# Kernel optimization log

Measured on AMD Instinct MI355X. Metric: run time of the kernel, lower is better.

The kernel has to match this reference:

```python
import math
import jax, jax.numpy as jnp
import numpy as np

B, T, HIDDEN = 2, 2048, 1024
H, HKV, D = 16, 16, 64


def _rope_tables(T, D):
    inv_freq = 1.0 / (10000.0 ** (jnp.arange(0, D, 2, dtype=jnp.float32) / D))
    t = jnp.arange(T, dtype=jnp.float32)
    freqs = jnp.outer(t, inv_freq)               # [T, D/2]
    emb = jnp.concatenate([freqs, freqs], axis=-1)  # [T, D]
    return jnp.cos(emb), jnp.sin(emb)


def setup_inputs() -> dict:
    key = jax.random.key(0)
    k1, k2, k3 = jax.random.split(key, 3)
    hidden_states = jax.random.normal(k1, (B, T, HIDDEN), dtype=jnp.float32)
    cos, sin = _rope_tables(T, D)
    # trunc-normal-ish init, std = 1/sqrt(fan_in)
    w_qkv = jax.random.normal(k2, ((H + 2 * HKV) * D, HIDDEN), dtype=jnp.float32) / math.sqrt(HIDDEN)
    w_o = jax.random.normal(k3, (HIDDEN, H * D), dtype=jnp.float32) / math.sqrt(H * D)
    return {"hidden_states": hidden_states, "cos": cos, "sin": sin, "w_qkv": w_qkv, "w_o": w_o}


def _rotate_half(x):
    x1, x2 = jnp.split(x, 2, axis=-1)
    return jnp.concatenate([-x2, x1], axis=-1)


def reference(hidden_states, cos, sin, w_qkv, w_o):
    b, t, _ = hidden_states.shape
    # fused QKV projection: [B,T,(H+2*HKV)*D]
    qkv = jnp.einsum('bti,oi->bto', hidden_states, w_qkv)
    qkv = qkv.reshape(b, t, H + 2 * HKV, D)
    q = qkv[:, :, :H]                    # [B,T,H,D]
    k = qkv[:, :, H:H + HKV]             # [B,T,HKV,D]
    v = qkv[:, :, H + HKV:]              # [B,T,HKV,D]
    # inline RoPE; cos/sin broadcast over heads
    c = cos[:, None, :]
    s = sin[:, None, :]
    q = q * c + _rotate_half(q) * s
    k = k * c + _rotate_half(k) * s
    scale = 1.0 / math.sqrt(D)
    attn_scores = jnp.einsum('bthd,bThd->bhtT', q, k) * scale  # [B,H,T,T]
    mask = jnp.tril(jnp.ones((t, t), dtype=bool))
    attn_scores = jnp.where(mask[None, None, :, :], attn_scores, -1e9)
    attn = jax.nn.softmax(attn_scores, axis=-1)
    context = jnp.einsum('bhtT,bThd->bthd', attn, v).reshape(b, t, H * D)
    return jnp.einsum('bti,oi->bto', context, w_o)
```

## Files before the change

kernel.cpp:

```cpp
#include <hip/hip_runtime.h>

typedef __bf16 bf16_t;
typedef __bf16 bf16x4 __attribute__((ext_vector_type(4)));
typedef __bf16 bf16x8 __attribute__((ext_vector_type(8)));
typedef float f32x4 __attribute__((ext_vector_type(4)));
typedef unsigned int u32x2 __attribute__((ext_vector_type(2)));
typedef unsigned long long u64;

#define MFMA16(a, b, c) __builtin_amdgcn_mfma_f32_16x16x32_bf16((a), (b), (c), 0, 0, 0)

#define LDG2LDS16(g, l)                                                        \
    __builtin_amdgcn_global_load_lds(                                          \
        (const __attribute__((address_space(1))) void*)(g),                    \
        (__attribute__((address_space(3))) void*)(l), 16, 0, 0)

#if __has_builtin(__builtin_amdgcn_exp2f)
#define EXP2(x) __builtin_amdgcn_exp2f(x)
#else
#define EXP2(x) exp2f(x)
#endif

__device__ inline bf16x8 load8(const float* p) {
    const f32x4 a = *(const f32x4*)p;
    const f32x4 b = *(const f32x4*)(p + 4);
    bf16x8 r;
#pragma unroll
    for (int i = 0; i < 4; i++) { r[i] = (bf16_t)a[i]; r[4 + i] = (bf16_t)b[i]; }
    return r;
}

__device__ inline u32x2 as2(bf16x4 v) {
    u32x2 r;
    __builtin_memcpy(&r, &v, 8);
    return r;
}

__device__ inline bf16x4 shfl4(bf16x4 v, int src) {
    u64 x;
    __builtin_memcpy(&x, &v, 8);
    x = __shfl(x, src, 64);
    bf16x4 r;
    __builtin_memcpy(&r, &x, 8);
    return r;
}

__global__ __launch_bounds__(256) void convert_kernel(const float* __restrict__ hs,
                                                      const float* __restrict__ wqkv,
                                                      const float* __restrict__ wo,
                                                      bf16_t* __restrict__ outb) {
    const size_t c = ((size_t)blockIdx.x * 256 + threadIdx.x) * 8;
    const float* src;
    size_t off;
    if (c < 4194304) { src = hs; off = c; }
    else if (c < 7340032) { src = wqkv; off = c - 4194304; }
    else { src = wo; off = c - 7340032; }
    *(bf16x8*)(outb + c) = load8(src + off);
}


template <int MODE, int NDIM, int BM>
__global__ __launch_bounds__(256) void gemm_bt(const bf16_t* __restrict__ A,
                                               const bf16_t* __restrict__ B,
                                               float* __restrict__ outp,
                                               bf16_t* __restrict__ q_ws,
                                               bf16_t* __restrict__ k_ws,
                                               bf16_t* __restrict__ v_ws,
                                               const float* __restrict__ cosb,
                                               const float* __restrict__ sinb) {
    constexpr int K = 1024;
    constexpr int IM = BM / 32;
    __shared__ __align__(16) bf16_t As[BM * 32];
    __shared__ __align__(16) bf16_t Bs[128 * 32];

    const int tid = threadIdx.x;
    const int w = tid >> 6;
    const int lane = tid & 63;
    const int lr = lane & 15;
    const int quad = lane >> 4;
    const int m0 = blockIdx.y * BM;
    const int n0 = blockIdx.x * 128;
    const int wm = (w & 1) * (BM / 2);
    const int wn = (w >> 1) * 64;

    const int srow = tid >> 2;
    const int skk = (tid & 3) * 8;
    const bf16_t* gA0 = A + (size_t)(m0 + srow) * K + skk;
    const bf16_t* gA1 = gA0 + (size_t)64 * K;
    const bf16_t* gB0 = B + (size_t)(n0 + srow) * K + skk;
    const bf16_t* gB1 = gB0 + (size_t)64 * K;
    bf16_t* lA0 = As + w * 512;
    bf16_t* lA1 = As + 2048 + w * 512;
    bf16_t* lB0 = Bs + w * 512;
    bf16_t* lB1 = Bs + 2048 + w * 512;

    f32x4 acc[IM][4] = {};

    for (int k0 = 0; k0 < K; k0 += 32) {
        LDG2LDS16(gA0 + k0, lA0);
        if constexpr (BM == 128) LDG2LDS16(gA1 + k0, lA1);
        LDG2LDS16(gB0 + k0, lB0);
        LDG2LDS16(gB1 + k0, lB1);
        __syncthreads();

        bf16x8 af[IM], bfm[4];
#pragma unroll
        for (int im = 0; im < IM; im++)
            af[im] = *(const bf16x8*)&As[(wm + im * 16 + lr) * 32 + quad * 8];
#pragma unroll
        for (int in = 0; in < 4; in++)
            bfm[in] = *(const bf16x8*)&Bs[(wn + in * 16 + lr) * 32 + quad * 8];
#pragma unroll
        for (int im = 0; im < IM; im++)
#pragma unroll
            for (int in = 0; in < 4; in++)
                acc[im][in] = MFMA16(af[im], bfm[in], acc[im][in]);
        __syncthreads();
    }

    if constexpr (MODE == 0) {
#pragma unroll
        for (int im = 0; im < IM; im++)
#pragma unroll
            for (int in = 0; in < 4; in++)
#pragma unroll
                for (int r = 0; r < 4; r++) {
                    const int m = m0 + wm + im * 16 + quad * 4 + r;
                    const int n = n0 + wn + in * 16 + lr;
                    outp[(size_t)m * NDIM + n] = acc[im][in][r];
                }
    } else {
        const int j = (n0 + wn) >> 6;
        if (j < 32) {
            const bool isq = (j < 16);
            const float qs = 0.125f * 1.44269504089f;
#pragma unroll
            for (int im = 0; im < IM; im++) {
#pragma unroll
                for (int r = 0; r < 4; r++) {
                    const int m = m0 + wm + im * 16 + quad * 4 + r;
                    const int b = m >> 11;
                    const int t = m & 2047;
#pragma unroll
                    for (int in = 0; in < 2; in++) {
                        const int d = in * 16 + lr;
                        const float x1 = acc[im][in][r];
                        const float x2 = acc[im][in + 2][r];
                        const float c = cosb[t * 64 + d];
                        const float s = sinb[t * 64 + d];
                        float y1 = x1 * c - x2 * s;
                        float y2 = x2 * c + x1 * s;
                        if (isq) {
                            y1 *= qs; y2 *= qs;
                            const size_t base =
                                ((size_t)(b * 16 + j) * 2048 + t) * 64 + d;
                            q_ws[base] = (bf16_t)y1;
                            q_ws[base + 32] = (bf16_t)y2;
                        } else {
                            const int bh = b * 16 + (j - 16);
                            const size_t off =
                                ((size_t)(bh * 128 + (t >> 4)) * 2) * 512 +
                                ((t & 15) + (d >> 3) * 16) * 8 + (d & 7);
                            k_ws[off] = (bf16_t)y1;
                            k_ws[off + 512] = (bf16_t)y2;
                        }
                    }
                }
            }
        } else {
#pragma unroll
            for (int im = 0; im < IM; im++)
#pragma unroll
                for (int in = 0; in < 4; in++)
#pragma unroll
                    for (int r = 0; r < 4; r++) {
                        const int m = m0 + wm + im * 16 + quad * 4 + r;
                        const int b = m >> 11;
                        const int t = m & 2047;
                        const int d = in * 16 + lr;
                        const int bh = b * 16 + (j - 32);
                        const size_t off =
                            ((size_t)(bh * 64 + (t >> 5)) * 4 + (d >> 4)) * 512 +
                            ((d & 15) + ((t & 31) >> 3) * 16) * 8 + (t & 7);
                        v_ws[off] = (bf16_t)acc[im][in][r];
                    }
        }
    }
}

__device__ inline void flash_tile(int qt, int quad, int lr, int query,
                                  const bf16_t* __restrict__ kbase,
                                  const bf16_t* __restrict__ vbase,
                                  bf16x8 qlo, bf16x8 qhi,
                                  f32x4* o, float& lrun) {
    bf16x8 kc[8];
#pragma unroll
    for (int n = 0; n < 4; n++) {
        kc[2 * n] = *(const bf16x8*)(kbase + (size_t)(n * 2) * 512);
        kc[2 * n + 1] = *(const bf16x8*)(kbase + (size_t)(n * 2 + 1) * 512);
    }

    for (int kb = 0; kb <= qt; kb++) {
        bf16x8 vv[2][4];
#pragma unroll
        for (int hh = 0; hh < 2; hh++)
#pragma unroll
            for (int n = 0; n < 4; n++)
                vv[hh][n] = *(const bf16x8*)(vbase +
                    (size_t)((kb * 2 + hh) * 4 + n) * 512);

        const int kbn = (kb < qt) ? kb + 1 : kb;
        bf16x8 kn[8];
#pragma unroll
        for (int n = 0; n < 4; n++) {
            kn[2 * n] = *(const bf16x8*)(kbase + (size_t)((kbn * 4 + n) * 2) * 512);
            kn[2 * n + 1] = *(const bf16x8*)(kbase + (size_t)((kbn * 4 + n) * 2 + 1) * 512);
        }

        const int u0 = kb * 64;
        f32x4 s[4];
#pragma unroll
        for (int n = 0; n < 4; n++) {
            const f32x4 z = {};
            s[n] = MFMA16(kc[2 * n], qlo, z);
            s[n] = MFMA16(kc[2 * n + 1], qhi, s[n]);
        }

        if (kb == qt) {
#pragma unroll
            for (int n = 0; n < 4; n++)
#pragma unroll
                for (int r = 0; r < 4; r++)
                    if (u0 + n * 16 + quad * 4 + r > query) s[n][r] = -1e9f;
        }

        f32x4 p[4];
#pragma unroll
        for (int n = 0; n < 4; n++)
#pragma unroll
            for (int r = 0; r < 4; r++) p[n][r] = EXP2(s[n][r]);

        lrun += ((p[0][0] + p[0][1]) + (p[0][2] + p[0][3])) +
                ((p[1][0] + p[1][1]) + (p[1][2] + p[1][3])) +
                ((p[2][0] + p[2][1]) + (p[2][2] + p[2][3])) +
                ((p[3][0] + p[3][1]) + (p[3][2] + p[3][3]));

        bf16x4 pb[4];
#pragma unroll
        for (int n = 0; n < 4; n++)
#pragma unroll
            for (int r = 0; r < 4; r++) pb[n][r] = (bf16_t)p[n][r];

#pragma unroll
        for (int hh = 0; hh < 2; hh++) {
            bf16x8 pf;
#if __has_builtin(__builtin_amdgcn_permlane16_swap) && \
    __has_builtin(__builtin_amdgcn_permlane32_swap)
            const u32x2 P0 = as2(pb[2 * hh]);
            const u32x2 P1 = as2(pb[2 * hh + 1]);
            const u32x2 s1a = __builtin_amdgcn_permlane16_swap(P0[0], P0[1], false, false);
            const u32x2 s1b = __builtin_amdgcn_permlane16_swap(P1[0], P1[1], false, false);
            const u32x2 s2a = __builtin_amdgcn_permlane32_swap(s1a[0], s1b[0], false, false);
            const u32x2 s2b = __builtin_amdgcn_permlane32_swap(s1a[1], s1b[1], false, false);
            const u32x2 s3a = __builtin_amdgcn_permlane16_swap(s2a[0], s2a[1], false, false);
            const u32x2 s3b = __builtin_amdgcn_permlane16_swap(s2b[0], s2b[1], false, false);
            const unsigned pfd[4] = {s3a[0], s3a[1], s3b[0], s3b[1]};
            __builtin_memcpy(&pf, pfd, 16);
#else
            const int srcLow = ((quad & 1) << 5) + lr;
            const int srcHigh = srcLow + 16;
            const bool loSel = (quad < 2);
            const bf16x4 a0 = shfl4(pb[2 * hh], srcLow);
            const bf16x4 a1 = shfl4(pb[2 * hh + 1], srcLow);
            const bf16x4 b0 = shfl4(pb[2 * hh], srcHigh);
            const bf16x4 b1 = shfl4(pb[2 * hh + 1], srcHigh);
            const bf16x4 lo = loSel ? a0 : a1;
            const bf16x4 hi = loSel ? b0 : b1;
#pragma unroll
            for (int r = 0; r < 4; r++) { pf[r] = lo[r]; pf[4 + r] = hi[r]; }
#endif
#pragma unroll
            for (int n = 0; n < 4; n++)
                o[n] = MFMA16(vv[hh][n], pf, o[n]);
        }

#pragma unroll
        for (int i = 0; i < 8; i++) kc[i] = kn[i];
    }
}

__global__ __launch_bounds__(256) void attn_kernel(const bf16_t* __restrict__ q_ws,
                                                   const bf16_t* __restrict__ k_ws,
                                                   const bf16_t* __restrict__ v_ws,
                                                   bf16_t* __restrict__ ctx) {
    const int tid = threadIdx.x;
    const int w = tid >> 6;
    const int lane = tid & 63;
    const int lr = lane & 15;
    const int quad = lane >> 4;
    const int bh = blockIdx.x & 31;
    const int pr = blockIdx.x >> 5;
    const int b = bh >> 4;
    const int hd = bh & 15;

    const bf16_t* kbase = k_ws + (size_t)bh * 131072 + lane * 8;
    const bf16_t* vbase = v_ws + (size_t)bh * 131072 + lane * 8;

#pragma unroll
    for (int half = 0; half < 2; half++) {
        const int qt = half ? (31 - pr) : pr;
        const int trow = qt * 64 + w * 16;
        const int query = trow + lr;

        const bf16_t* qb = q_ws + ((size_t)bh * 2048 + trow + lr) * 64 + quad * 8;
        const bf16x8 qlo = *(const bf16x8*)qb;
        const bf16x8 qhi = *(const bf16x8*)(qb + 32);

        f32x4 o[4] = {};
        float lrun = 0.0f;
        flash_tile(qt, quad, lr, query, kbase, vbase, qlo, qhi, o, lrun);

        lrun += __shfl_xor(lrun, 16);
        lrun += __shfl_xor(lrun, 32);

        const float inv = 1.0f / fmaxf(lrun, 1e-30f);
        const size_t base = ((size_t)b * 2048 + query) * 1024 + hd * 64 + quad * 4;
#pragma unroll
        for (int n = 0; n < 4; n++) {
            bf16x4 ob;
#pragma unroll
            for (int r = 0; r < 4; r++) ob[r] = (bf16_t)(o[n][r] * inv);
            *(bf16x4*)&ctx[base + n * 16] = ob;
        }
    }
}

extern "C" void kernel_launch(void* const* d_in, const int* in_sizes, int n_in,
                              void* d_out, int out_size, void* d_ws, size_t ws_size,
                              hipStream_t stream) {
    const float* hs = (const float*)d_in[0];
    const float* cosb = (const float*)d_in[1];
    const float* sinb = (const float*)d_in[2];
    const float* wqkv = (const float*)d_in[3];
    const float* wo = (const float*)d_in[4];
    float* out = (float*)d_out;

    char* ws = (char*)d_ws;
    bf16_t* hs_b = (bf16_t*)(ws);
    bf16_t* wqkv_b = hs_b + 4194304;
    bf16_t* wo_b = hs_b + 7340032;
    bf16_t* q_ws = (bf16_t*)(ws + (size_t)(16u << 20));
    bf16_t* k_ws = (bf16_t*)(ws + (size_t)(24u << 20));
    bf16_t* v_ws = (bf16_t*)(ws + (size_t)(32u << 20));
    bf16_t* ctx = (bf16_t*)(ws);

    const dim3 blk(256);

    convert_kernel<<<dim3(4096), blk, 0, stream>>>(hs, wqkv, wo, hs_b);

    gemm_bt<1, 3072, 128><<<dim3(24, 32), blk, 0, stream>>>(
        hs_b, wqkv_b, nullptr, q_ws, k_ws, v_ws, cosb, sinb);

    attn_kernel<<<dim3(512), blk, 0, stream>>>(q_ws, k_ws, v_ws, ctx);

    gemm_bt<0, 1024, 64><<<dim3(8, 64), blk, 0, stream>>>(
        ctx, wo_b, out, nullptr, nullptr, nullptr, nullptr, nullptr);
}
```

Before: 178.0 us.

## Process two query row-tiles per wave to reuse K/V loads in attention

Attention blocks now use 2 waves of 128 threads, and each wave computes two 16-row query tiles against the same K/V fragments. This halves K/V global loads per query row. The old scheme paired a short and a long causal tile in one block for load balance; now each block handles one 64-row tile, with 1024 blocks ordered longest-first. The cost is higher register pressure and possibly lower occupancy.

```diff
diff --git a/kernel.cpp b/kernel.cpp
--- a/kernel.cpp
+++ b/kernel.cpp
@@ -42,6 +42,36 @@
     bf16x4 r;
     __builtin_memcpy(&r, &x, 8);
     return r;
+}
+
+__device__ inline bf16x8 ptrans(bf16x4 pA, bf16x4 pB, int quad, int lr) {
+    bf16x8 pf;
+#if __has_builtin(__builtin_amdgcn_permlane16_swap) && \
+    __has_builtin(__builtin_amdgcn_permlane32_swap)
+    const u32x2 P0 = as2(pA);
+    const u32x2 P1 = as2(pB);
+    const u32x2 s1a = __builtin_amdgcn_permlane16_swap(P0[0], P0[1], false, false);
+    const u32x2 s1b = __builtin_amdgcn_permlane16_swap(P1[0], P1[1], false, false);
+    const u32x2 s2a = __builtin_amdgcn_permlane32_swap(s1a[0], s1b[0], false, false);
+    const u32x2 s2b = __builtin_amdgcn_permlane32_swap(s1a[1], s1b[1], false, false);
+    const u32x2 s3a = __builtin_amdgcn_permlane16_swap(s2a[0], s2a[1], false, false);
+    const u32x2 s3b = __builtin_amdgcn_permlane16_swap(s2b[0], s2b[1], false, false);
+    const unsigned pfd[4] = {s3a[0], s3a[1], s3b[0], s3b[1]};
+    __builtin_memcpy(&pf, pfd, 16);
+#else
+    const int srcLow = ((quad & 1) << 5) + lr;
+    const int srcHigh = srcLow + 16;
+    const bool loSel = (quad < 2);
+    const bf16x4 a0 = shfl4(pA, srcLow);
+    const bf16x4 a1 = shfl4(pB, srcLow);
+    const bf16x4 b0 = shfl4(pA, srcHigh);
+    const bf16x4 b1 = shfl4(pB, srcHigh);
+    const bf16x4 lo = loSel ? a0 : a1;
+    const bf16x4 hi = loSel ? b0 : b1;
+#pragma unroll
+    for (int r = 0; r < 4; r++) { pf[r] = lo[r]; pf[4 + r] = hi[r]; }
+#endif
+    return pf;
 }
 
 __global__ __launch_bounds__(256) void convert_kernel(const float* __restrict__ hs,
@@ -187,108 +217,7 @@
     }
 }
 
-__device__ inline void flash_tile(int qt, int quad, int lr, int query,
-                                  const bf16_t* __restrict__ kbase,
-                                  const bf16_t* __restrict__ vbase,
-                                  bf16x8 qlo, bf16x8 qhi,
-                                  f32x4* o, float& lrun) {
-    bf16x8 kc[8];
-#pragma unroll
-    for (int n = 0; n < 4; n++) {
-        kc[2 * n] = *(const bf16x8*)(kbase + (size_t)(n * 2) * 512);
-        kc[2 * n + 1] = *(const bf16x8*)(kbase + (size_t)(n * 2 + 1) * 512);
-    }
-
-    for (int kb = 0; kb <= qt; kb++) {
-        bf16x8 vv[2][4];
-#pragma unroll
-        for (int hh = 0; hh < 2; hh++)
-#pragma unroll
-            for (int n = 0; n < 4; n++)
-                vv[hh][n] = *(const bf16x8*)(vbase +
-                    (size_t)((kb * 2 + hh) * 4 + n) * 512);
-
-        const int kbn = (kb < qt) ? kb + 1 : kb;
-        bf16x8 kn[8];
-#pragma unroll
-        for (int n = 0; n < 4; n++) {
-            kn[2 * n] = *(const bf16x8*)(kbase + (size_t)((kbn * 4 + n) * 2) * 512);
-            kn[2 * n + 1] = *(const bf16x8*)(kbase + (size_t)((kbn * 4 + n) * 2 + 1) * 512);
-        }
-
-        const int u0 = kb * 64;
-        f32x4 s[4];
-#pragma unroll
-        for (int n = 0; n < 4; n++) {
-            const f32x4 z = {};
-            s[n] = MFMA16(kc[2 * n], qlo, z);
-            s[n] = MFMA16(kc[2 * n + 1], qhi, s[n]);
-        }
-
-        if (kb == qt) {
-#pragma unroll
-            for (int n = 0; n < 4; n++)
-#pragma unroll
-                for (int r = 0; r < 4; r++)
-                    if (u0 + n * 16 + quad * 4 + r > query) s[n][r] = -1e9f;
-        }
-
-        f32x4 p[4];
-#pragma unroll
-        for (int n = 0; n < 4; n++)
-#pragma unroll
-            for (int r = 0; r < 4; r++) p[n][r] = EXP2(s[n][r]);
-
-        lrun += ((p[0][0] + p[0][1]) + (p[0][2] + p[0][3])) +
-                ((p[1][0] + p[1][1]) + (p[1][2] + p[1][3])) +
-                ((p[2][0] + p[2][1]) + (p[2][2] + p[2][3])) +
-                ((p[3][0] + p[3][1]) + (p[3][2] + p[3][3]));
-
-        bf16x4 pb[4];
-#pragma unroll
-        for (int n = 0; n < 4; n++)
-#pragma unroll
-            for (int r = 0; r < 4; r++) pb[n][r] = (bf16_t)p[n][r];
-
-#pragma unroll
-        for (int hh = 0; hh < 2; hh++) {
-            bf16x8 pf;
-#if __has_builtin(__builtin_amdgcn_permlane16_swap) && \
-    __has_builtin(__builtin_amdgcn_permlane32_swap)
-            const u32x2 P0 = as2(pb[2 * hh]);
-            const u32x2 P1 = as2(pb[2 * hh + 1]);
-            const u32x2 s1a = __builtin_amdgcn_permlane16_swap(P0[0], P0[1], false, false);
-            const u32x2 s1b = __builtin_amdgcn_permlane16_swap(P1[0], P1[1], false, false);
-            const u32x2 s2a = __builtin_amdgcn_permlane32_swap(s1a[0], s1b[0], false, false);
-            const u32x2 s2b = __builtin_amdgcn_permlane32_swap(s1a[1], s1b[1], false, false);
-            const u32x2 s3a = __builtin_amdgcn_permlane16_swap(s2a[0], s2a[1], false, false);
-            const u32x2 s3b = __builtin_amdgcn_permlane16_swap(s2b[0], s2b[1], false, false);
-            const unsigned pfd[4] = {s3a[0], s3a[1], s3b[0], s3b[1]};
-            __builtin_memcpy(&pf, pfd, 16);
-#else
-            const int srcLow = ((quad & 1) << 5) + lr;
-            const int srcHigh = srcLow + 16;
-            const bool loSel = (quad < 2);
-            const bf16x4 a0 = shfl4(pb[2 * hh], srcLow);
-            const bf16x4 a1 = shfl4(pb[2 * hh + 1], srcLow);
-            const bf16x4 b0 = shfl4(pb[2 * hh], srcHigh);
-            const bf16x4 b1 = shfl4(pb[2 * hh + 1], srcHigh);
-            const bf16x4 lo = loSel ? a0 : a1;
-            const bf16x4 hi = loSel ? b0 : b1;
-#pragma unroll
-            for (int r = 0; r < 4; r++) { pf[r] = lo[r]; pf[4 + r] = hi[r]; }
-#endif
-#pragma unroll
-            for (int n = 0; n < 4; n++)
-                o[n] = MFMA16(vv[hh][n], pf, o[n]);
-        }
-
-#pragma unroll
-        for (int i = 0; i < 8; i++) kc[i] = kn[i];
-    }
-}
-
-__global__ __launch_bounds__(256) void attn_kernel(const bf16_t* __restrict__ q_ws,
+__global__ __launch_bounds__(128) void attn_kernel(const bf16_t* __restrict__ q_ws,
                                                    const bf16_t* __restrict__ k_ws,
                                                    const bf16_t* __restrict__ v_ws,
                                                    bf16_t* __restrict__ ctx) {
@@ -298,39 +227,123 @@
     const int lr = lane & 15;
     const int quad = lane >> 4;
     const int bh = blockIdx.x & 31;
-    const int pr = blockIdx.x >> 5;
+    const int qt = 31 - (blockIdx.x >> 5);
     const int b = bh >> 4;
     const int hd = bh & 15;
+    const int trow0 = qt * 64 + w * 32;
+    const int trow1 = trow0 + 16;
+    const int query0 = trow0 + lr;
+    const int query1 = trow1 + lr;
 
     const bf16_t* kbase = k_ws + (size_t)bh * 131072 + lane * 8;
     const bf16_t* vbase = v_ws + (size_t)bh * 131072 + lane * 8;
 
-#pragma unroll
-    for (int half = 0; half < 2; half++) {
-        const int qt = half ? (31 - pr) : pr;
-        const int trow = qt * 64 + w * 16;
-        const int query = trow + lr;
-
-        const bf16_t* qb = q_ws + ((size_t)bh * 2048 + trow + lr) * 64 + quad * 8;
-        const bf16x8 qlo = *(const bf16x8*)qb;
-        const bf16x8 qhi = *(const bf16x8*)(qb + 32);
-
-        f32x4 o[4] = {};
-        float lrun = 0.0f;
-        flash_tile(qt, quad, lr, query, kbase, vbase, qlo, qhi, o, lrun);
-
-        lrun += __shfl_xor(lrun, 16);
-        lrun += __shfl_xor(lrun, 32);
-
-        const float inv = 1.0f / fmaxf(lrun, 1e-30f);
-        const size_t base = ((size_t)b * 2048 + query) * 1024 + hd * 64 + quad * 4;
+    const bf16_t* qb0 = q_ws + ((size_t)bh * 2048 + query0) * 64 + quad * 8;
+    const bf16_t* qb1 = q_ws + ((size_t)bh * 2048 + query1) * 64 + quad * 8;
+    const bf16x8 q0lo = *(const bf16x8*)qb0;
+    const bf16x8 q0hi = *(const bf16x8*)(qb0 + 32);
+    const bf16x8 q1lo = *(const bf16x8*)qb1;
+    const bf16x8 q1hi = *(const bf16x8*)(qb1 + 32);
+
+    f32x4 o0[4] = {}, o1[4] = {};
+    float l0 = 0.0f, l1 = 0.0f;
+
+    bf16x8 kc[8];
+#pragma unroll
+    for (int n = 0; n < 4; n++) {
+        kc[2 * n] = *(const bf16x8*)(kbase + (size_t)(n * 2) * 512);
+        kc[2 * n + 1] = *(const bf16x8*)(kbase + (size_t)(n * 2 + 1) * 512);
+    }
+
+    for (int kb = 0; kb <= qt; kb++) {
+        bf16x8 vv[2][4];
+#pragma unroll
+        for (int hh = 0; hh < 2; hh++)
+#pragma unroll
+            for (int n = 0; n < 4; n++)
+                vv[hh][n] = *(const bf16x8*)(vbase +
+                    (size_t)((kb * 2 + hh) * 4 + n) * 512);
+
+        const int kbn = (kb < qt) ? kb + 1 : kb;
+        bf16x8 kn[8];
 #pragma unroll
         for (int n = 0; n < 4; n++) {
-            bf16x4 ob;
-#pragma unroll
-            for (int r = 0; r < 4; r++) ob[r] = (bf16_t)(o[n][r] * inv);
-            *(bf16x4*)&ctx[base + n * 16] = ob;
-        }
+            kn[2 * n] = *(const bf16x8*)(kbase + (size_t)((kbn * 4 + n) * 2) * 512);
+            kn[2 * n + 1] = *(const bf16x8*)(kbase + (size_t)((kbn * 4 + n) * 2 + 1) * 512);
+        }
+
+        const int u0 = kb * 64;
+        f32x4 s0[4], s1[4];
+#pragma unroll
+        for (int n = 0; n < 4; n++) {
+            const f32x4 z = {};
+            s0[n] = MFMA16(kc[2 * n], q0lo, z);
+            s0[n] = MFMA16(kc[2 * n + 1], q0hi, s0[n]);
+            s1[n] = MFMA16(kc[2 * n], q1lo, z);
+            s1[n] = MFMA16(kc[2 * n + 1], q1hi, s1[n]);
+        }
+
+        if (kb == qt) {
+#pragma unroll
+            for (int n = 0; n < 4; n++)
+#pragma unroll
+                for (int r = 0; r < 4; r++) {
+                    const int key = u0 + n * 16 + quad * 4 + r;
+                    if (key > query0) s0[n][r] = -1e9f;
+                    if (key > query1) s1[n][r] = -1e9f;
+                }
+        }
+
+        bf16x4 pb0[4], pb1[4];
+        float rs0 = 0.0f, rs1 = 0.0f;
+#pragma unroll
+        for (int n = 0; n < 4; n++) {
+#pragma unroll
+            for (int r = 0; r < 4; r++) {
+                const float e0 = EXP2(s0[n][r]);
+                const float e1 = EXP2(s1[n][r]);
+                rs0 += e0; rs1 += e1;
+                pb0[n][r] = (bf16_t)e0;
+                pb1[n][r] = (bf16_t)e1;
+            }
+        }
+        l0 += rs0;
+        l1 += rs1;
+
+#pragma unroll
+        for (int hh = 0; hh < 2; hh++) {
+            const bf16x8 pf0 = ptrans(pb0[2 * hh], pb0[2 * hh + 1], quad, lr);
+            const bf16x8 pf1 = ptrans(pb1[2 * hh], pb1[2 * hh + 1], quad, lr);
+#pragma unroll
+            for (int n = 0; n < 4; n++) {
+                o0[n] = MFMA16(vv[hh][n], pf0, o0[n]);
+                o1[n] = MFMA16(vv[hh][n], pf1, o1[n]);
+            }
+        }
+
+#pragma unroll
+        for (int i = 0; i < 8; i++) kc[i] = kn[i];
+    }
+
+    l0 += __shfl_xor(l0, 16);
+    l0 += __shfl_xor(l0, 32);
+    l1 += __shfl_xor(l1, 16);
+    l1 += __shfl_xor(l1, 32);
+
+    const float inv0 = 1.0f / fmaxf(l0, 1e-30f);
+    const float inv1 = 1.0f / fmaxf(l1, 1e-30f);
+    const size_t base0 = ((size_t)b * 2048 + query0) * 1024 + hd * 64 + quad * 4;
+    const size_t base1 = ((size_t)b * 2048 + query1) * 1024 + hd * 64 + quad * 4;
+#pragma unroll
+    for (int n = 0; n < 4; n++) {
+        bf16x4 ob0, ob1;
+#pragma unroll
+        for (int r = 0; r < 4; r++) {
+            ob0[r] = (bf16_t)(o0[n][r] * inv0);
+            ob1[r] = (bf16_t)(o1[n][r] * inv1);
+        }
+        *(bf16x4*)&ctx[base0 + n * 16] = ob0;
+        *(bf16x4*)&ctx[base1 + n * 16] = ob1;
     }
 }
 
@@ -353,15 +366,13 @@
     bf16_t* v_ws = (bf16_t*)(ws + (size_t)(32u << 20));
     bf16_t* ctx = (bf16_t*)(ws);
 
-    const dim3 blk(256);
-
-    convert_kernel<<<dim3(4096), blk, 0, stream>>>(hs, wqkv, wo, hs_b);
-
-    gemm_bt<1, 3072, 128><<<dim3(24, 32), blk, 0, stream>>>(
+    convert_kernel<<<dim3(4096), dim3(256), 0, stream>>>(hs, wqkv, wo, hs_b);
+
+    gemm_bt<1, 3072, 128><<<dim3(24, 32), dim3(256), 0, stream>>>(
         hs_b, wqkv_b, nullptr, q_ws, k_ws, v_ws, cosb, sinb);
 
-    attn_kernel<<<dim3(512), blk, 0, stream>>>(q_ws, k_ws, v_ws, ctx);
-
-    gemm_bt<0, 1024, 64><<<dim3(8, 64), blk, 0, stream>>>(
+    attn_kernel<<<dim3(1024), dim3(128), 0, stream>>>(q_ws, k_ws, v_ws, ctx);
+
+    gemm_bt<0, 1024, 64><<<dim3(8, 64), dim3(256), 0, stream>>>(
         ctx, wo_b, out, nullptr, nullptr, nullptr, nullptr, nullptr);
 }
```

Result: slower. 182.4 us (+2.5%).
